# Kernel tuning notes

Measured on AMD Instinct MI355X. Metric: run time of the kernel, lower is better.

## Reference

```python
import jax, jax.numpy as jnp
import numpy as np

B, C, P, NG, NCLS, HID, N, IMG = 2, 256, 7, 2, 81, 1024, 512, 800
STRIDES = [4, 8, 16, 32]
SCALE = 56.0  # roi_map_level_scale


def _roi_align(feat, rois, pooled, scale, ng):
    """torchvision-legacy (aligned=False) ROI Align. feat [B,C,H,W], rois [N,5]."""
    Bf, Cf, H, W = feat.shape
    ft = jnp.transpose(feat, (0, 2, 3, 1))  # [B,H,W,C]
    b = rois[:, 0].astype(jnp.int32)
    x1, y1, x2, y2 = (rois[:, i] * scale for i in (1, 2, 3, 4))
    rw = jnp.maximum(x2 - x1, 1.0)
    rh = jnp.maximum(y2 - y1, 1.0)
    # sample grid per output bin: ng points per axis, centered in sub-bins
    g = (jnp.arange(pooled)[:, None] + (jnp.arange(ng)[None, :] + 0.5) / ng).reshape(-1)  # [P*ng]
    ys = y1[:, None] + g[None, :] * (rh / pooled)[:, None]  # [N,S]
    xs = x1[:, None] + g[None, :] * (rw / pooled)[:, None]

    def axis(coord, size):
        valid = (coord >= -1.0) & (coord <= size)
        c = jnp.clip(coord, 0.0, size - 1)
        lo = jnp.floor(c).astype(jnp.int32)
        hi = jnp.minimum(lo + 1, size - 1)
        return valid, lo, hi, c - lo

    vy, ylo, yhi, fy = axis(ys, H)
    vx, xlo, xhi, fx = axis(xs, W)
    bb = b[:, None, None]

    def gather(yi, xi):
        return ft[bb, yi[:, :, None], xi[:, None, :], :]  # [N,S,S,C]

    wy = fy[:, :, None, None]
    wx = fx[:, None, :, None]
    val = ((1 - wy) * (1 - wx) * gather(ylo, xlo) + (1 - wy) * wx * gather(ylo, xhi)
           + wy * (1 - wx) * gather(yhi, xlo) + wy * wx * gather(yhi, xhi))
    val = jnp.where((vy[:, :, None] & vx[:, None, :])[..., None], val, 0.0)
    val = val.reshape(-1, pooled, ng, pooled, ng, Cf).mean(axis=(2, 4))  # [N,P,P,C]
    return jnp.transpose(val, (0, 3, 1, 2))  # [N,C,P,P]


def setup_inputs() -> dict:
    key = jax.random.key(0)
    ks = jax.random.split(key, 16)
    feats = {}
    for i, s in enumerate(STRIDES):
        hw = IMG // s
        feats[f"p{i+2}"] = jax.random.normal(ks[i], (B, C, hw, hw), jnp.float32)
    # realistic proposals: batch idx + boxes with sizes 16..512 px
    bidx = jax.random.randint(ks[4], (N,), 0, B).astype(jnp.float32)
    sw = 2.0 ** jax.random.uniform(ks[5], (N,), minval=4.0, maxval=9.0)
    sh = 2.0 ** jax.random.uniform(ks[6], (N,), minval=4.0, maxval=9.0)
    x1 = jax.random.uniform(ks[7], (N,)) * (IMG - sw)
    y1 = jax.random.uniform(ks[8], (N,)) * (IMG - sh)
    rois = jnp.stack([bidx, x1, y1, x1 + sw - 1, y1 + sh - 1], axis=1)
    D = C * P * P
    inp = dict(feats, rois=rois,
               w1=0.01 * jax.random.normal(ks[9], (HID, D), jnp.float32),
               b1=jnp.zeros((HID,), jnp.float32),
               w2=0.01 * jax.random.normal(ks[10], (HID, HID), jnp.float32),
               b2=jnp.zeros((HID,), jnp.float32),
               w_cls=0.01 * jax.random.normal(ks[11], (NCLS, HID), jnp.float32),
               b_cls=jnp.zeros((NCLS,), jnp.float32),
               w_reg=0.001 * jax.random.normal(ks[12], (NCLS * 4, HID), jnp.float32),
               b_reg=jnp.zeros((NCLS * 4,), jnp.float32))
    return inp


def reference(p2, p3, p4, p5, rois, w1, b1, w2, b2, w_cls, b_cls, w_reg, b_reg):
    feats = [p2, p3, p4, p5]
    # FPN level assignment (same math as torch: log2(sqrt(hw)/scale + 1e-6), floor, clamp)
    rh = rois[:, 4] - rois[:, 2] + 1
    rw = rois[:, 3] - rois[:, 1] + 1
    levels = jnp.clip(jnp.floor(jnp.log2(jnp.sqrt(rh * rw) / SCALE + 1e-6)), 0, 3).astype(jnp.int32)
    # dispatch: compute each ROI on its assigned level (masked combine == gather/sort-scatter)
    pooled = jnp.zeros((rois.shape[0], C, P, P), rois.dtype)
    for l, feat in enumerate(feats):
        pl = _roi_align(feat, rois, P, 1.0 / STRIDES[l], NG)
        pooled = pooled + jnp.where((levels == l)[:, None, None, None], pl, 0.0)
    x = pooled.reshape(pooled.shape[0], -1)  # [N, C*P*P]
    x = jax.nn.relu(x @ w1.T + b1)
    x = jax.nn.relu(x @ w2.T + b2)
    x_cls = x @ w_cls.T + b_cls
    x_reg = x @ w_reg.T + b_reg  # TEST mode, not class-agnostic: no gather
    cls_probs = jax.nn.softmax(x_cls, axis=1)
    rois_out = rois.reshape(B, -1, 5)
    cls_probs = cls_probs.reshape(B, rois_out.shape[1], -1)
    bbox_preds = x_reg.reshape(B, rois_out.shape[1], -1)
    return rois_out, cls_probs, bbox_preds
```

## Files before the change

kernel.cpp:

```cpp
#include <hip/hip_runtime.h>
#include <hip/hip_bf16.h>
#include <math.h>

#define NROI   512
#define CCH    256
#define POOLP  7
#define DDIM   12544
#define HIDN   1024
#define NCLS   81
#define NREG   324
#define NHEAD  512
#define OUT_ROIS   2560
#define OUT_CLS    (512*81)

typedef __attribute__((ext_vector_type(4))) float f32x4;
typedef __attribute__((ext_vector_type(8))) short bf16x8;

static __device__ __forceinline__ unsigned short f2bf(float x) {
    __hip_bfloat16 h = __float2bfloat16(x);
    return *reinterpret_cast<unsigned short*>(&h);
}
static __device__ __forceinline__ float bf2f(unsigned short u) {
    unsigned int b = ((unsigned int)u) << 16;
    return *reinterpret_cast<float*>(&b);
}

#define PS_B0 10
#define PS_B1 (PS_B0 + 256)
#define PS_B2 (PS_B1 + 1024)
#define PS_B3 (PS_B2 + 1024)
#define PS_B4 (PS_B3 + 1024)
__global__ __launch_bounds__(256) void prep_k(const float* __restrict__ rois,
                                              const float* __restrict__ w1,
                                              const float* __restrict__ w2,
                                              const float* __restrict__ wc,
                                              const float* __restrict__ wr,
                                              float* __restrict__ out,
                                              float* __restrict__ hf,
                                              unsigned short* __restrict__ w1b,
                                              unsigned short* __restrict__ w2b,
                                              unsigned short* __restrict__ whd) {
    __shared__ unsigned short lw[49 * 258];
    int bid = blockIdx.x, t = threadIdx.x;
    if (bid < PS_B0) {
        int i = bid * 256 + t;
        if (i < OUT_ROIS) out[i] = rois[i];
    } else if (bid < PS_B1) {
        int i = (bid - PS_B0) * 256 + t;
        ((float4*)hf)[i] = make_float4(0.f, 0.f, 0.f, 0.f);
    } else if (bid < PS_B2) {
        int i = (bid - PS_B1) * 256 + t;
        float4 v = ((const float4*)w2)[i];
        ushort4 o;
        o.x = f2bf(v.x); o.y = f2bf(v.y); o.z = f2bf(v.z); o.w = f2bf(v.w);
        ((ushort4*)w2b)[i] = o;
    } else if (bid < PS_B3) {
        int i2 = (bid - PS_B2) * 256 + t;
        int r = i2 >> 9, c = (i2 & 511) << 1;
        float v0, v1;
        if (r < NCLS)             { v0 = wc[r * HIDN + c]; v1 = wc[r * HIDN + c + 1]; }
        else if (r < NCLS + NREG) { v0 = wr[(r - NCLS) * HIDN + c]; v1 = wr[(r - NCLS) * HIDN + c + 1]; }
        else                      { v0 = 0.f; v1 = 0.f; }
        ((unsigned int*)whd)[i2] = (unsigned int)f2bf(v0) | ((unsigned int)f2bf(v1) << 16);
    } else {
        int n = bid - PS_B3;
        const float* src = w1 + (size_t)n * DDIM;
        for (int k = t; k < DDIM; k += 256) {
            int c = k / 49;
            int s = k - c * 49;
            lw[s * 258 + c] = f2bf(src[k]);
        }
        __syncthreads();
        unsigned int* dst = (unsigned int*)(w1b + (size_t)n * DDIM);
        for (int j2 = t; j2 < DDIM / 2; j2 += 256) {
            int s = j2 >> 7, c2 = (j2 & 127) << 1;
            dst[j2] = lw[s * 258 + c2] | ((unsigned int)lw[s * 258 + c2 + 1] << 16);
        }
    }
}

__global__ __launch_bounds__(256) void transpose_k(const float* __restrict__ p2,
                                                   const float* __restrict__ p3,
                                                   const float* __restrict__ p4,
                                                   const float* __restrict__ p5,
                                                   unsigned short* __restrict__ f0,
                                                   unsigned short* __restrict__ f1,
                                                   unsigned short* __restrict__ f2,
                                                   unsigned short* __restrict__ f3) {
    __shared__ unsigned short sm[128][66];
    int idx = blockIdx.x;
    const float* in; unsigned short* op; int S, base;
    if (idx < 313)      { in = p2; op = f0; S = 40000; base = 0; }
    else if (idx < 392) { in = p3; op = f1; S = 10000; base = 313; }
    else if (idx < 412) { in = p4; op = f2; S = 2500;  base = 392; }
    else                { in = p5; op = f3; S = 625;   base = 412; }
    int s0 = (idx - base) * 128;
    int c0 = blockIdx.y * 64;
    int b  = blockIdx.z;
    int t  = threadIdx.x;

    int k = t & 31, g = t >> 5;
    bool vec = (s0 + 128 <= S);
#pragma unroll
    for (int jj = 0; jj < 8; jj++) {
        int c = g + jj * 8;
        const float* src = in + ((size_t)(b * CCH + c0 + c)) * S + s0 + k * 4;
        if (vec) {
            float4 v = *(const float4*)src;
#pragma unroll
            for (int e = 0; e < 4; e++) {
                int s = k * 4 + e;
                float val = (e == 0) ? v.x : (e == 1) ? v.y : (e == 2) ? v.z : v.w;
                sm[s][c ^ ((s & 7) << 3)] = f2bf(val);
            }
        } else {
#pragma unroll
            for (int e = 0; e < 4; e++) {
                int s = k * 4 + e;
                sm[s][c ^ ((s & 7) << 3)] =
                    (s0 + s < S) ? f2bf(src[e]) : (unsigned short)0;
            }
        }
    }
    __syncthreads();

    int lane = t & 63, w = t >> 6;
    int rl = lane >> 4, cw = (lane & 15) * 4;
#pragma unroll
    for (int i = 0; i < 8; i++) {
        int s = w * 32 + i * 4 + rl;
        if (s0 + s < S) {
            int sw = (s & 7) << 3;
            unsigned short u0 = sm[s][(cw + 0) ^ sw];
            unsigned short u1 = sm[s][(cw + 1) ^ sw];
            unsigned short u2 = sm[s][(cw + 2) ^ sw];
            unsigned short u3 = sm[s][(cw + 3) ^ sw];
            uint2 v;
            v.x = (unsigned int)u0 | ((unsigned int)u1 << 16);
            v.y = (unsigned int)u2 | ((unsigned int)u3 << 16);
            *(uint2*)(op + ((size_t)b * S + s0 + s) * CCH + c0 + cw) = v;
        }
    }
}

__global__ __launch_bounds__(256) void roi_align_k(const unsigned short* __restrict__ f0,
                                                   const unsigned short* __restrict__ f1,
                                                   const unsigned short* __restrict__ f2,
                                                   const unsigned short* __restrict__ f3,
                                                   const float* __restrict__ rois,
                                                   unsigned short* __restrict__ xpool) {
    __shared__ float s_f[16];
    __shared__ int   s_lo[16], s_hi[16], s_v[16];

    int py = blockIdx.x, r = blockIdx.y, t = threadIdx.x;

    float r0  = rois[r * 5 + 0];
    float rx1 = rois[r * 5 + 1], ry1 = rois[r * 5 + 2];
    float rx2 = rois[r * 5 + 3], ry2 = rois[r * 5 + 4];
    int b = (int)r0;

    float aw = rx2 - rx1 + 1.f, ah = ry2 - ry1 + 1.f;
    float lvf = floorf(log2f(sqrtf(ah * aw) / 56.f + 1e-6f));
    int lv = (int)fminf(fmaxf(lvf, 0.f), 3.f);

    const unsigned short* F = (lv == 0) ? f0 : (lv == 1) ? f1 : (lv == 2) ? f2 : f3;
    int HW      = (lv == 0) ? 200 : (lv == 1) ? 100 : (lv == 2) ? 50 : 25;
    float scale = (lv == 0) ? 0.25f : (lv == 1) ? 0.125f : (lv == 2) ? 0.0625f : 0.03125f;

    float x1 = rx1 * scale, yy1 = ry1 * scale;
    float x2 = rx2 * scale, yy2 = ry2 * scale;
    float rw = fmaxf(x2 - x1, 1.f), rh = fmaxf(yy2 - yy1, 1.f);

    if (t < 16) {
        bool isY = t < 2;
        float coord;
        if (isY) {
            float g = (float)py + ((float)t + 0.5f) * 0.5f;
            coord = yy1 + g * (rh * (1.f / 7.f));
        } else {
            int j = t - 2;
            float g = (float)(j >> 1) + ((float)(j & 1) + 0.5f) * 0.5f;
            coord = x1 + g * (rw * (1.f / 7.f));
        }
        int vld = (coord >= -1.f && coord <= (float)HW) ? 1 : 0;
        float c = fminf(fmaxf(coord, 0.f), (float)(HW - 1));
        int lo  = (int)floorf(c);
        int hi  = min(lo + 1, HW - 1);
        s_v[t] = vld; s_lo[t] = lo; s_hi[t] = hi; s_f[t] = c - (float)lo;
    }
    __syncthreads();

    const unsigned short* Fb = F + ((size_t)b * HW * HW) * CCH + t;
    size_t obase = (size_t)r * DDIM + py * 7 * 256 + t;

    for (int px = 0; px < POOLP; px++) {
        float acc = 0.f;
#pragma unroll
        for (int s = 0; s < 4; s++) {
            int iy = s >> 1;
            int ix = px * 2 + (s & 1);
            int vy = s_v[iy], vx = s_v[2 + ix];
            if (vy & vx) {
                float fy = s_f[iy], fx = s_f[2 + ix];
                int ylo = s_lo[iy], yhi = s_hi[iy];
                int xlo = s_lo[2 + ix], xhi = s_hi[2 + ix];
                float v00 = bf2f(Fb[((size_t)ylo * HW + xlo) * CCH]);
                float v01 = bf2f(Fb[((size_t)ylo * HW + xhi) * CCH]);
                float v10 = bf2f(Fb[((size_t)yhi * HW + xlo) * CCH]);
                float v11 = bf2f(Fb[((size_t)yhi * HW + xhi) * CCH]);
                acc += (1.f - fy) * ((1.f - fx) * v00 + fx * v01)
                     + fy * ((1.f - fx) * v10 + fx * v11);
            }
        }
        xpool[obase + px * 256] = f2bf(acc * 0.25f);
    }
}

__global__ __launch_bounds__(256) void roi_align_nchw_k(const float* __restrict__ f0,
                                                        const float* __restrict__ f1,
                                                        const float* __restrict__ f2,
                                                        const float* __restrict__ f3,
                                                        const float* __restrict__ rois,
                                                        unsigned short* __restrict__ xpool) {
    __shared__ float s_f[16];
    __shared__ int   s_lo[16], s_hi[16], s_v[16];
    int py = blockIdx.x, r = blockIdx.y, t = threadIdx.x;
    float r0  = rois[r * 5 + 0];
    float rx1 = rois[r * 5 + 1], ry1 = rois[r * 5 + 2];
    float rx2 = rois[r * 5 + 3], ry2 = rois[r * 5 + 4];
    int b = (int)r0;
    float aw = rx2 - rx1 + 1.f, ah = ry2 - ry1 + 1.f;
    float lvf = floorf(log2f(sqrtf(ah * aw) / 56.f + 1e-6f));
    int lv = (int)fminf(fmaxf(lvf, 0.f), 3.f);
    const float* F = (lv == 0) ? f0 : (lv == 1) ? f1 : (lv == 2) ? f2 : f3;
    int HW      = (lv == 0) ? 200 : (lv == 1) ? 100 : (lv == 2) ? 50 : 25;
    float scale = (lv == 0) ? 0.25f : (lv == 1) ? 0.125f : (lv == 2) ? 0.0625f : 0.03125f;
    float x1 = rx1 * scale, yy1 = ry1 * scale;
    float x2 = rx2 * scale, yy2 = ry2 * scale;
    float rw = fmaxf(x2 - x1, 1.f), rh = fmaxf(yy2 - yy1, 1.f);
    if (t < 16) {
        bool isY = t < 2;
        float coord;
        if (isY) {
            float g = (float)py + ((float)t + 0.5f) * 0.5f;
            coord = yy1 + g * (rh * (1.f / 7.f));
        } else {
            int j = t - 2;
            float g = (float)(j >> 1) + ((float)(j & 1) + 0.5f) * 0.5f;
            coord = x1 + g * (rw * (1.f / 7.f));
        }
        int vld = (coord >= -1.f && coord <= (float)HW) ? 1 : 0;
        float c = fminf(fmaxf(coord, 0.f), (float)(HW - 1));
        int lo  = (int)floorf(c);
        int hi  = min(lo + 1, HW - 1);
        s_v[t] = vld; s_lo[t] = lo; s_hi[t] = hi; s_f[t] = c - (float)lo;
    }
    __syncthreads();
    const float* Fb = F + ((size_t)b * CCH + t) * HW * HW;
    size_t obase = (size_t)r * DDIM + py * 7 * 256 + t;
    for (int px = 0; px < POOLP; px++) {
        float acc = 0.f;
#pragma unroll
        for (int s = 0; s < 4; s++) {
            int iy = s >> 1, ix = px * 2 + (s & 1);
            int vy = s_v[iy], vx = s_v[2 + ix];
            if (vy & vx) {
                float fy = s_f[iy], fx = s_f[2 + ix];
                int ylo = s_lo[iy], yhi = s_hi[iy];
                int xlo = s_lo[2 + ix], xhi = s_hi[2 + ix];
                float v00 = Fb[(size_t)ylo * HW + xlo];
                float v01 = Fb[(size_t)ylo * HW + xhi];
                float v10 = Fb[(size_t)yhi * HW + xlo];
                float v11 = Fb[(size_t)yhi * HW + xhi];
                acc += (1.f - fy) * ((1.f - fx) * v00 + fx * v01)
                     + fy * ((1.f - fx) * v10 + fx * v11);
            }
        }
        xpool[obase + px * 256] = f2bf(acc * 0.25f);
    }
}

__global__ __launch_bounds__(256) void gemm_bf16_k(const unsigned short* __restrict__ A,
                                                   const unsigned short* __restrict__ W,
                                                   float* __restrict__ Cacc,
                                                   int M, int N, int K, int kchunk) {
    __shared__ __align__(16) unsigned short As[2][8][64][8];
    __shared__ __align__(16) unsigned short Ws[2][8][64][8];

    int t = threadIdx.x;
    int lane = t & 63, wid = t >> 6;
    int m0 = blockIdx.y * 64, n0 = blockIdx.x * 64;
    int k0 = blockIdx.z * kchunk;
    int wm = (wid >> 1) * 32, wn = (wid & 1) * 32;
    int fr = lane & 15, kg = lane >> 4;
    int nsteps = kchunk >> 6;

    f32x4 acc[2][2] = {};

    const unsigned short* Arow = A + (size_t)(m0 + lane) * K;
    const unsigned short* Wrow = W + (size_t)(n0 + lane) * K;

    auto stage = [&](int buf, int kb) {
#pragma unroll
        for (int i = 0; i < 2; i++) {
            int c = wid * 2 + i;
            __builtin_amdgcn_global_load_lds(
                (const __attribute__((address_space(1))) void*)(Arow + kb + c * 8),
                (__attribute__((address_space(3))) void*)(&As[buf][c][0][0]), 16, 0, 0);
            __builtin_amdgcn_global_load_lds(
                (const __attribute__((address_space(1))) void*)(Wrow + kb + c * 8),
                (__attribute__((address_space(3))) void*)(&Ws[buf][c][0][0]), 16, 0, 0);
        }
    };

    stage(0, k0);
    __syncthreads();
    int cur = 0;
    for (int tt = 0; tt < nsteps; ++tt) {
        if (tt + 1 < nsteps) stage(cur ^ 1, k0 + (tt + 1) * 64);
#pragma unroll
        for (int h = 0; h < 2; h++) {
            bf16x8 a0 = *(const bf16x8*)(&As[cur][h * 4 + kg][wm + fr][0]);
            bf16x8 a1 = *(const bf16x8*)(&As[cur][h * 4 + kg][wm + 16 + fr][0]);
            bf16x8 b0 = *(const bf16x8*)(&Ws[cur][h * 4 + kg][wn + fr][0]);
            bf16x8 b1 = *(const bf16x8*)(&Ws[cur][h * 4 + kg][wn + 16 + fr][0]);
            acc[0][0] = __builtin_amdgcn_mfma_f32_16x16x32_bf16(a0, b0, acc[0][0], 0, 0, 0);
            acc[0][1] = __builtin_amdgcn_mfma_f32_16x16x32_bf16(a0, b1, acc[0][1], 0, 0, 0);
            acc[1][0] = __builtin_amdgcn_mfma_f32_16x16x32_bf16(a1, b0, acc[1][0], 0, 0, 0);
            acc[1][1] = __builtin_amdgcn_mfma_f32_16x16x32_bf16(a1, b1, acc[1][1], 0, 0, 0);
        }
        __syncthreads();
        cur ^= 1;
    }

    int row = m0 + wm + (lane >> 4) * 4;
    int col = n0 + wn + fr;
#pragma unroll
    for (int fm = 0; fm < 2; fm++)
#pragma unroll
        for (int fn = 0; fn < 2; fn++)
#pragma unroll
            for (int r = 0; r < 4; r++)
                atomicAdd(&Cacc[(size_t)(row + fm * 16 + r) * N + col + fn * 16],
                          acc[fm][fn][r]);
}

__global__ __launch_bounds__(256) void gemm_fc2_k(const unsigned short* __restrict__ A,
                                                  const unsigned short* __restrict__ W,
                                                  const float* __restrict__ bias,
                                                  unsigned short* __restrict__ dst,
                                                  int M, int N, int K) {
    __shared__ __align__(16) unsigned short As[2][8][64][8];
    __shared__ __align__(16) unsigned short Ws[2][8][64][8];

    int t = threadIdx.x;
    int lane = t & 63, wid = t >> 6;
    int m0 = blockIdx.y * 64, n0 = blockIdx.x * 64;
    int wm = (wid >> 1) * 32, wn = (wid & 1) * 32;
    int fr = lane & 15, kg = lane >> 4;
    int nsteps = K >> 6;

    f32x4 acc[2][2] = {};

    const unsigned short* Arow = A + (size_t)(m0 + lane) * K;
    const unsigned short* Wrow = W + (size_t)(n0 + lane) * K;

    auto stage = [&](int buf, int kb) {
#pragma unroll
        for (int i = 0; i < 2; i++) {
            int c = wid * 2 + i;
            __builtin_amdgcn_global_load_lds(
                (const __attribute__((address_space(1))) void*)(Arow + kb + c * 8),
                (__attribute__((address_space(3))) void*)(&As[buf][c][0][0]), 16, 0, 0);
            __builtin_amdgcn_global_load_lds(
                (const __attribute__((address_space(1))) void*)(Wrow + kb + c * 8),
                (__attribute__((address_space(3))) void*)(&Ws[buf][c][0][0]), 16, 0, 0);
        }
    };

    stage(0, 0);
    __syncthreads();
    int cur = 0;
    for (int tt = 0; tt < nsteps; ++tt) {
        if (tt + 1 < nsteps) stage(cur ^ 1, (tt + 1) * 64);
#pragma unroll
        for (int h = 0; h < 2; h++) {
            bf16x8 a0 = *(const bf16x8*)(&As[cur][h * 4 + kg][wm + fr][0]);
            bf16x8 a1 = *(const bf16x8*)(&As[cur][h * 4 + kg][wm + 16 + fr][0]);
            bf16x8 b0 = *(const bf16x8*)(&Ws[cur][h * 4 + kg][wn + fr][0]);
            bf16x8 b1 = *(const bf16x8*)(&Ws[cur][h * 4 + kg][wn + 16 + fr][0]);
            acc[0][0] = __builtin_amdgcn_mfma_f32_16x16x32_bf16(a0, b0, acc[0][0], 0, 0, 0);
            acc[0][1] = __builtin_amdgcn_mfma_f32_16x16x32_bf16(a0, b1, acc[0][1], 0, 0, 0);
            acc[1][0] = __builtin_amdgcn_mfma_f32_16x16x32_bf16(a1, b0, acc[1][0], 0, 0, 0);
            acc[1][1] = __builtin_amdgcn_mfma_f32_16x16x32_bf16(a1, b1, acc[1][1], 0, 0, 0);
        }
        __syncthreads();
        cur ^= 1;
    }

    int row = m0 + wm + (lane >> 4) * 4;
    int col = n0 + wn + fr;
#pragma unroll
    for (int fm = 0; fm < 2; fm++)
#pragma unroll
        for (int fn = 0; fn < 2; fn++) {
            float bv = bias[col + fn * 16];
#pragma unroll
            for (int r = 0; r < 4; r++) {
                float v = fmaxf(acc[fm][fn][r] + bv, 0.f);
                dst[(size_t)(row + fm * 16 + r) * N + col + fn * 16] = f2bf(v);
            }
        }
}

__global__ __launch_bounds__(256) void gemm128_bf16_k(const unsigned short* __restrict__ A,
                                                      const unsigned short* __restrict__ W,
                                                      float* __restrict__ Cp,
                                                      int M, int N, int K, int kchunk) {
    __shared__ __align__(16) unsigned short As[2][8][64][8];
    __shared__ __align__(16) unsigned short Ws[2][8][128][8];

    int lin  = blockIdx.x;
    int nb   = (lin & 7) * 112 + (lin >> 3);
    int tile = nb / 14, bz = nb - tile * 14;
    int bx = tile >> 3, by = tile & 7;

    int t = threadIdx.x;
    int lane = t & 63, wid = t >> 6;
    int m0 = by * 64, n0 = bx * 128;
    int k0 = bz * kchunk;
    int wm = (wid >> 1) * 32, wn = (wid & 1) * 64;
    int fr = lane & 15, kg = lane >> 4;
    int nsteps = kchunk >> 6;

    f32x4 acc[2][4] = {};

    const unsigned short* Arow = A + (size_t)(m0 + lane) * K;

    auto stage = [&](int buf, int kb) {
#pragma unroll
        for (int i = 0; i < 6; i++) {
            int c = wid * 6 + i;
            if (c < 8) {
                __builtin_amdgcn_global_load_lds(
                    (const __attribute__((address_space(1))) void*)(Arow + kb + c * 8),
                    (__attribute__((address_space(3))) void*)(&As[buf][c][0][0]), 16, 0, 0);
            } else {
                int idx = c - 8, kgc = idx & 7, rh = idx >> 3;
                __builtin_amdgcn_global_load_lds(
                    (const __attribute__((address_space(1))) void*)
                        (W + (size_t)(n0 + rh * 64 + lane) * K + kb + kgc * 8),
                    (__attribute__((address_space(3))) void*)(&Ws[buf][kgc][rh * 64][0]),
                    16, 0, 0);
            }
        }
    };

    stage(0, k0);
    __syncthreads();
    int cur = 0;
    for (int tt = 0; tt < nsteps; ++tt) {
        if (tt + 1 < nsteps) stage(cur ^ 1, k0 + (tt + 1) * 64);
#pragma unroll
        for (int h = 0; h < 2; h++) {
            bf16x8 av[2], bv[4];
#pragma unroll
            for (int f = 0; f < 2; f++)
                av[f] = *(const bf16x8*)(&As[cur][h * 4 + kg][wm + f * 16 + fr][0]);
#pragma unroll
            for (int f = 0; f < 4; f++)
                bv[f] = *(const bf16x8*)(&Ws[cur][h * 4 + kg][wn + f * 16 + fr][0]);
#pragma unroll
            for (int fm = 0; fm < 2; fm++)
#pragma unroll
                for (int fn = 0; fn < 4; fn++)
                    acc[fm][fn] = __builtin_amdgcn_mfma_f32_16x16x32_bf16(
                        av[fm], bv[fn], acc[fm][fn], 0, 0, 0);
        }
        __syncthreads();
        cur ^= 1;
    }

    float* Cout = Cp + (size_t)bz * ((size_t)M * N);
    int row = m0 + wm + (lane >> 4) * 4;
    int col = n0 + wn + fr;
#pragma unroll
    for (int fm = 0; fm < 2; fm++)
#pragma unroll
        for (int fn = 0; fn < 4; fn++)
#pragma unroll
            for (int r = 0; r < 4; r++)
                Cout[(size_t)(row + fm * 16 + r) * N + col + fn * 16] = acc[fm][fn][r];
}

__global__ __launch_bounds__(256) void fc_ep_k(const float* __restrict__ Cp,
                                               const float* __restrict__ bias,
                                               unsigned short* __restrict__ dst,
                                               int MN, int ks) {
    int i = blockIdx.x * 256 + threadIdx.x;
    if (i >= MN) return;
    float s = 0.f;
    for (int p = 0; p < ks; p++) s += Cp[(size_t)p * MN + i];
    s = fmaxf(s + bias[i & (HIDN - 1)], 0.f);
    dst[i] = f2bf(s);
}

__global__ void head_ep_k(const float* __restrict__ hf,
                          const float* __restrict__ bc,
                          const float* __restrict__ br,
                          float* __restrict__ out) {
    int r = blockIdx.x, l = threadIdx.x;
    const float* row = hf + (size_t)r * NHEAD;

    float* reg = out + OUT_ROIS + OUT_CLS + (size_t)r * NREG;
    for (int j = l; j < NREG; j += 64) reg[j] = row[NCLS + j] + br[j];

    float v0 = row[l] + bc[l];
    float v1 = (l + 64 < NCLS) ? row[l + 64] + bc[l + 64] : -INFINITY;
    float m = fmaxf(v0, v1);
#pragma unroll
    for (int o = 32; o; o >>= 1) m = fmaxf(m, __shfl_xor(m, o));
    float e0 = __expf(v0 - m);
    float e1 = (l + 64 < NCLS) ? __expf(v1 - m) : 0.f;
    float s = e0 + e1;
#pragma unroll
    for (int o = 32; o; o >>= 1) s += __shfl_xor(s, o);
    float inv = 1.f / s;
    float* cls = out + OUT_ROIS + (size_t)r * NCLS;
    cls[l] = e0 * inv;
    if (l + 64 < NCLS) cls[l + 64] = e1 * inv;
}

extern "C" void kernel_launch(void* const* d_in, const int* in_sizes, int n_in,
                              void* d_out, int out_size, void* d_ws, size_t ws_size,
                              hipStream_t stream) {
    const float* p2   = (const float*)d_in[0];
    const float* p3   = (const float*)d_in[1];
    const float* p4   = (const float*)d_in[2];
    const float* p5   = (const float*)d_in[3];
    const float* rois = (const float*)d_in[4];
    const float* w1   = (const float*)d_in[5];
    const float* b1   = (const float*)d_in[6];
    const float* w2   = (const float*)d_in[7];
    const float* b2   = (const float*)d_in[8];
    const float* wc   = (const float*)d_in[9];
    const float* bc   = (const float*)d_in[10];
    const float* wr   = (const float*)d_in[11];
    const float* br   = (const float*)d_in[12];

    float* out = (float*)d_out;

    const int KS1 = 14;

    char* p = (char*)d_ws;
    auto alloc = [&](size_t bytes) { char* r = p; p += (bytes + 255) & ~(size_t)255; return r; };
    unsigned short* xpool = (unsigned short*)alloc((size_t)NROI * DDIM * 2);
    unsigned short* y1b   = (unsigned short*)alloc((size_t)NROI * HIDN * 2);
    unsigned short* y2b   = (unsigned short*)alloc((size_t)NROI * HIDN * 2);
    unsigned short* w1b   = (unsigned short*)alloc((size_t)HIDN * DDIM * 2);
    unsigned short* w2b   = (unsigned short*)alloc((size_t)HIDN * HIDN * 2);
    unsigned short* whd   = (unsigned short*)alloc((size_t)NHEAD * HIDN * 2);
    float*          hf    = (float*)alloc((size_t)NROI * NHEAD * 4);
    unsigned short* ft0 = (unsigned short*)alloc((size_t)2 * 40000 * CCH * 2);
    unsigned short* ft1 = (unsigned short*)alloc((size_t)2 * 10000 * CCH * 2);
    unsigned short* ft2 = (unsigned short*)alloc((size_t)2 * 2500 * CCH * 2);
    unsigned short* ft3 = (unsigned short*)alloc((size_t)2 * 625 * CCH * 2);
    bool nhwc = (size_t)(p - (char*)d_ws) <= ws_size;

    float* part = (float*)ft0;

    prep_k<<<PS_B4, 256, 0, stream>>>(rois, w1, w2, wc, wr, out, hf, w1b, w2b, whd);

    if (nhwc) {
        transpose_k<<<dim3(417, 4, 2), 256, 0, stream>>>(p2, p3, p4, p5,
                                                         ft0, ft1, ft2, ft3);
        roi_align_k<<<dim3(POOLP, NROI), 256, 0, stream>>>(ft0, ft1, ft2, ft3, rois, xpool);
    } else {
        roi_align_nchw_k<<<dim3(POOLP, NROI), 256, 0, stream>>>(p2, p3, p4, p5, rois, xpool);
    }

    gemm128_bf16_k<<<8 * 8 * KS1, 256, 0, stream>>>(
        xpool, w1b, part, NROI, HIDN, DDIM, DDIM / KS1);
    fc_ep_k<<<(NROI * HIDN + 255) / 256, 256, 0, stream>>>(part, b1, y1b, NROI * HIDN, KS1);

    gemm_fc2_k<<<dim3(HIDN / 64, NROI / 64), 256, 0, stream>>>(
        y1b, w2b, b2, y2b, NROI, HIDN, HIDN);

    gemm_bf16_k<<<dim3(NHEAD / 64, NROI / 64, 4), 256, 0, stream>>>(
        y2b, whd, hf, NROI, NHEAD, HIDN, HIDN / 4);
    head_ep_k<<<NROI, 64, 0, stream>>>(hf, bc, br, out);
}
```

Measured before the change: 180.5 us.

## Use 128x128 tiles, 28-way split-K with bf16 partials for FC1

The FC1 GEMM grows its tile from 64x128 to 128x128 per block, drops LDS double buffering in favour of a single buffer, and raises split-K from 14 to 28 chunks so the grid stays at 896 blocks. Partial sums are stored as bf16 instead of fp32, which halves partial-buffer traffic, and the reduction epilogue is vectorised to handle four elements per thread. The larger tile improves operand reuse per MFMA. In exchange it loses load/compute overlap, and rounding each of 28 partials to bf16 before summing adds error.

```diff
diff --git a/kernel.cpp b/kernel.cpp
--- a/kernel.cpp
+++ b/kernel.cpp
@@ -415,94 +415,91 @@
 
 __global__ __launch_bounds__(256) void gemm128_bf16_k(const unsigned short* __restrict__ A,
                                                       const unsigned short* __restrict__ W,
-                                                      float* __restrict__ Cp,
+                                                      unsigned short* __restrict__ Cp,
                                                       int M, int N, int K, int kchunk) {
-    __shared__ __align__(16) unsigned short As[2][8][64][8];
-    __shared__ __align__(16) unsigned short Ws[2][8][128][8];
+    __shared__ __align__(16) unsigned short As[8][128][8];
+    __shared__ __align__(16) unsigned short Ws[8][128][8];
 
     int lin  = blockIdx.x;
     int nb   = (lin & 7) * 112 + (lin >> 3);
-    int tile = nb / 14, bz = nb - tile * 14;
-    int bx = tile >> 3, by = tile & 7;
+    int tile = nb / 28, bz = nb - tile * 28;
+    int bx = tile & 7, by = tile >> 3;
 
     int t = threadIdx.x;
     int lane = t & 63, wid = t >> 6;
-    int m0 = by * 64, n0 = bx * 128;
+    int m0 = by * 128, n0 = bx * 128;
     int k0 = bz * kchunk;
-    int wm = (wid >> 1) * 32, wn = (wid & 1) * 64;
+    int wm = (wid >> 1) * 64, wn = (wid & 1) * 64;
     int fr = lane & 15, kg = lane >> 4;
-    int nsteps = kchunk >> 6;
-
-    f32x4 acc[2][4] = {};
-
-    const unsigned short* Arow = A + (size_t)(m0 + lane) * K;
-
-    auto stage = [&](int buf, int kb) {
-#pragma unroll
-        for (int i = 0; i < 6; i++) {
-            int c = wid * 6 + i;
-            if (c < 8) {
-                __builtin_amdgcn_global_load_lds(
-                    (const __attribute__((address_space(1))) void*)(Arow + kb + c * 8),
-                    (__attribute__((address_space(3))) void*)(&As[buf][c][0][0]), 16, 0, 0);
-            } else {
-                int idx = c - 8, kgc = idx & 7, rh = idx >> 3;
-                __builtin_amdgcn_global_load_lds(
-                    (const __attribute__((address_space(1))) void*)
-                        (W + (size_t)(n0 + rh * 64 + lane) * K + kb + kgc * 8),
-                    (__attribute__((address_space(3))) void*)(&Ws[buf][kgc][rh * 64][0]),
-                    16, 0, 0);
+
+    f32x4 acc[4][4] = {};
+
+    for (int kb = k0; kb < k0 + kchunk; kb += 64) {
+#pragma unroll
+        for (int i = 0; i < 4; i++) {
+            int c   = wid * 4 + i;
+            int kgc = c >> 1;
+            int r0w = (c & 1) * 64;
+            __builtin_amdgcn_global_load_lds(
+                (const __attribute__((address_space(1))) void*)
+                    (A + (size_t)(m0 + r0w + lane) * K + kb + kgc * 8),
+                (__attribute__((address_space(3))) void*)(&As[kgc][r0w][0]), 16, 0, 0);
+            __builtin_amdgcn_global_load_lds(
+                (const __attribute__((address_space(1))) void*)
+                    (W + (size_t)(n0 + r0w + lane) * K + kb + kgc * 8),
+                (__attribute__((address_space(3))) void*)(&Ws[kgc][r0w][0]), 16, 0, 0);
+        }
+        __syncthreads();
+#pragma unroll
+        for (int h = 0; h < 2; h++) {
+            bf16x8 av[4], bv[4];
+#pragma unroll
+            for (int f = 0; f < 4; f++) {
+                av[f] = *(const bf16x8*)(&As[h * 4 + kg][wm + f * 16 + fr][0]);
+                bv[f] = *(const bf16x8*)(&Ws[h * 4 + kg][wn + f * 16 + fr][0]);
             }
-        }
-    };
-
-    stage(0, k0);
-    __syncthreads();
-    int cur = 0;
-    for (int tt = 0; tt < nsteps; ++tt) {
-        if (tt + 1 < nsteps) stage(cur ^ 1, k0 + (tt + 1) * 64);
-#pragma unroll
-        for (int h = 0; h < 2; h++) {
-            bf16x8 av[2], bv[4];
-#pragma unroll
-            for (int f = 0; f < 2; f++)
-                av[f] = *(const bf16x8*)(&As[cur][h * 4 + kg][wm + f * 16 + fr][0]);
-#pragma unroll
-            for (int f = 0; f < 4; f++)
-                bv[f] = *(const bf16x8*)(&Ws[cur][h * 4 + kg][wn + f * 16 + fr][0]);
-#pragma unroll
-            for (int fm = 0; fm < 2; fm++)
+#pragma unroll
+            for (int fm = 0; fm < 4; fm++)
 #pragma unroll
                 for (int fn = 0; fn < 4; fn++)
                     acc[fm][fn] = __builtin_amdgcn_mfma_f32_16x16x32_bf16(
                         av[fm], bv[fn], acc[fm][fn], 0, 0, 0);
         }
         __syncthreads();
-        cur ^= 1;
-    }
-
-    float* Cout = Cp + (size_t)bz * ((size_t)M * N);
+    }
+
+    unsigned short* Cout = Cp + (size_t)bz * ((size_t)M * N);
     int row = m0 + wm + (lane >> 4) * 4;
     int col = n0 + wn + fr;
 #pragma unroll
-    for (int fm = 0; fm < 2; fm++)
+    for (int fm = 0; fm < 4; fm++)
 #pragma unroll
         for (int fn = 0; fn < 4; fn++)
 #pragma unroll
             for (int r = 0; r < 4; r++)
-                Cout[(size_t)(row + fm * 16 + r) * N + col + fn * 16] = acc[fm][fn][r];
-}
-
-__global__ __launch_bounds__(256) void fc_ep_k(const float* __restrict__ Cp,
-                                               const float* __restrict__ bias,
-                                               unsigned short* __restrict__ dst,
-                                               int MN, int ks) {
+                Cout[(size_t)(row + fm * 16 + r) * N + col + fn * 16] =
+                    f2bf(acc[fm][fn][r]);
+}
+
+__global__ __launch_bounds__(256) void fc_ep28_k(const unsigned short* __restrict__ Cp,
+                                                 const float* __restrict__ bias,
+                                                 unsigned short* __restrict__ dst,
+                                                 int ks) {
+    const int MN = NROI * HIDN;
     int i = blockIdx.x * 256 + threadIdx.x;
-    if (i >= MN) return;
-    float s = 0.f;
-    for (int p = 0; p < ks; p++) s += Cp[(size_t)p * MN + i];
-    s = fmaxf(s + bias[i & (HIDN - 1)], 0.f);
-    dst[i] = f2bf(s);
+    size_t base = (size_t)i * 4;
+    float s0 = 0.f, s1 = 0.f, s2 = 0.f, s3 = 0.f;
+    for (int p = 0; p < ks; p++) {
+        ushort4 u = *(const ushort4*)(Cp + (size_t)p * MN + base);
+        s0 += bf2f(u.x); s1 += bf2f(u.y); s2 += bf2f(u.z); s3 += bf2f(u.w);
+    }
+    int col = (int)(base & (HIDN - 1));
+    ushort4 o;
+    o.x = f2bf(fmaxf(s0 + bias[col + 0], 0.f));
+    o.y = f2bf(fmaxf(s1 + bias[col + 1], 0.f));
+    o.z = f2bf(fmaxf(s2 + bias[col + 2], 0.f));
+    o.w = f2bf(fmaxf(s3 + bias[col + 3], 0.f));
+    *(ushort4*)(dst + base) = o;
 }
 
 __global__ void head_ep_k(const float* __restrict__ hf,
@@ -550,7 +547,7 @@
 
     float* out = (float*)d_out;
 
-    const int KS1 = 14;
+    const int KS1 = 28;
 
     char* p = (char*)d_ws;
     auto alloc = [&](size_t bytes) { char* r = p; p += (bytes + 255) & ~(size_t)255; return r; };
@@ -567,7 +564,7 @@
     unsigned short* ft3 = (unsigned short*)alloc((size_t)2 * 625 * CCH * 2);
     bool nhwc = (size_t)(p - (char*)d_ws) <= ws_size;
 
-    float* part = (float*)ft0;
+    unsigned short* part = ft0;
 
     prep_k<<<PS_B4, 256, 0, stream>>>(rois, w1, w2, wc, wr, out, hf, w1b, w2b, whd);
 
@@ -579,9 +576,9 @@
         roi_align_nchw_k<<<dim3(POOLP, NROI), 256, 0, stream>>>(p2, p3, p4, p5, rois, xpool);
     }
 
-    gemm128_bf16_k<<<8 * 8 * KS1, 256, 0, stream>>>(
+    gemm128_bf16_k<<<8 * 4 * KS1, 256, 0, stream>>>(
         xpool, w1b, part, NROI, HIDN, DDIM, DDIM / KS1);
-    fc_ep_k<<<(NROI * HIDN + 255) / 256, 256, 0, stream>>>(part, b1, y1b, NROI * HIDN, KS1);
+    fc_ep28_k<<<(NROI * HIDN / 4 + 255) / 256, 256, 0, stream>>>(part, b1, y1b, KS1);
 
     gemm_fc2_k<<<dim3(HIDN / 64, NROI / 64), 256, 0, stream>>>(
         y1b, w2b, b2, y2b, NROI, HIDN, HIDN);
```

Result: faster. 167.7 us (-7.1%).
